# Optimization experiments

Measured on AMD Instinct MI355X. Metric: run time of the kernel, lower is better.

## Reference

```python
import jax, jax.numpy as jnp
import numpy as np
from jax import lax

NOISE_STD = 0.05
TAU = 0.2
B, T, I, H = 16, 512, 8, 256


def setup_inputs() -> dict:
    key = jax.random.key(0)
    ks = jax.random.split(key, 6)
    u = jax.random.normal(ks[0], (B, T, I), dtype=jnp.float32)
    x0 = jnp.zeros((B, H), dtype=jnp.float32)
    noise = jax.random.normal(ks[1], (T, B, H), dtype=jnp.float32)
    # nn.init.normal_(w_hh, std=0.1/H)
    w_hh = jax.random.normal(ks[2], (H, H, H), dtype=jnp.float32) * (0.1 / H)
    # nn.init.normal_(w_in.weight), zero bias
    w_in_w = jax.random.normal(ks[3], (H, I), dtype=jnp.float32)
    w_in_b = jnp.zeros((H,), dtype=jnp.float32)
    # default nn.Linear init for w_out (uniform), approximated with scaled uniform
    bound = 1.0 / np.sqrt(H)
    w_out_w = jax.random.uniform(ks[4], (I, H), dtype=jnp.float32, minval=-bound, maxval=bound)
    w_out_b = jax.random.uniform(ks[5], (I,), dtype=jnp.float32, minval=-bound, maxval=bound)
    return {"u": u, "x0": x0, "noise": noise, "w_hh": w_hh,
            "w_in_w": w_in_w, "w_in_b": w_in_b, "w_out_w": w_out_w, "w_out_b": w_out_b}


def reference(u, x0, noise, w_hh, w_in_w, w_in_b, w_out_w, w_out_b):
    # Precompute input projection for all timesteps: [B,T,H] -> [T,B,H]
    inp = jnp.einsum('bti,hi->tbh', u, w_in_w) + w_in_b

    def step(x, ts):
        u_proj, n_t = ts                     # [B,H], [B,H]
        r = jnp.tanh(x)                      # form='rate'
        # bilinear recurrence: einsum('bj,ijk,bk->bi', r, w_hh, r)
        tmp = jnp.einsum('ijk,bk->bij', w_hh, r)   # [B,H,H]
        rec = jnp.einsum('bj,bij->bi', r, tmp)     # [B,H]
        rec_x = rec + u_proj
        x_new = x + NOISE_STD * n_t + TAU * (-x + rec_x)  # mode='cont'
        return x_new, x_new

    x_last, traj_tb = lax.scan(step, x0, (inp, noise))
    traj = jnp.swapaxes(traj_tb, 0, 1)       # [B,T,H]
    output = jnp.einsum('bth,oh->bto', jnp.tanh(traj), w_out_w) + w_out_b
    return output, x_last, traj
```

## Files before the change

### kernel.cpp

```cpp
#include <hip/hip_runtime.h>
#include <hip/hip_fp16.h>
#include <stdint.h>


#define NOISE_STD 0.05f
#define TAU 0.2f

typedef _Float16 f16x8 __attribute__((ext_vector_type(8)));
typedef float f32x4 __attribute__((ext_vector_type(4)));
typedef unsigned int u32x4 __attribute__((ext_vector_type(4)));

__device__ __forceinline__ float fast_tanh(float x){
  float cx = fminf(fmaxf(x, -10.f), 10.f);
  float e = __expf(2.f*cx);
  return 1.f - 2.f*__builtin_amdgcn_rcpf(e + 1.f);
}

__device__ __forceinline__ void block_sync_lds(){
  asm volatile("s_waitcnt lgkmcnt(0)\n\ts_barrier" ::: "memory");
}

__device__ __forceinline__ unsigned pkmax_u16(unsigned a, unsigned b){
  unsigned d;
  asm("v_pk_max_u16 %0, %1, %2" : "=v"(d) : "v"(a), "v"(b));
  return d;
}

__device__ __forceinline__ bool pair_bad(u32x4 a, u32x4 b){
  unsigned m = pkmax_u16(pkmax_u16(pkmax_u16(a.x, a.y), pkmax_u16(a.z, a.w)),
                         pkmax_u16(pkmax_u16(b.x, b.y), pkmax_u16(b.z, b.w)));
  return ((m & 0xFFFFu) == 0xFFFFu) || ((m >> 16) == 0xFFFFu);
}

__device__ __forceinline__ float row16_sum(float v){
  float s = v; int t;
  t = __builtin_amdgcn_update_dpp(__float_as_int(s), __float_as_int(s), 0x121, 0xF, 0xF, false); s += __int_as_float(t);
  t = __builtin_amdgcn_update_dpp(__float_as_int(s), __float_as_int(s), 0x122, 0xF, 0xF, false); s += __int_as_float(t);
  t = __builtin_amdgcn_update_dpp(__float_as_int(s), __float_as_int(s), 0x124, 0xF, 0xF, false); s += __int_as_float(t);
  t = __builtin_amdgcn_update_dpp(__float_as_int(s), __float_as_int(s), 0x128, 0xF, 0xF, false); s += __int_as_float(t);
  return s;
}

__device__ __forceinline__ unsigned pack2h(float a, float b){
  return (unsigned)__half_as_ushort(__float2half(a)) |
         ((unsigned)__half_as_ushort(__float2half(b)) << 16);
}

__global__ void prep_kernel(const float* __restrict__ u, const float* __restrict__ noise,
                            const float* __restrict__ w_in_w, const float* __restrict__ w_in_b,
                            const float* __restrict__ w_hh,
                            float* __restrict__ pre2, __half* __restrict__ wsw,
                            uint4* __restrict__ rG4, int sent_u4){
  int F = blockIdx.x*256 + threadIdx.x;
  {
    int b = F & 15; int h = (F>>4) & 255; int t = F >> 12;
    const float* up = u + (b*512 + t)*8;
    const float* wp = w_in_w + h*8;
    float s = w_in_b[h];
    #pragma unroll
    for (int i2 = 0; i2 < 8; ++i2) s += up[i2]*wp[i2];
    pre2[h*8192 + t*16 + b] = NOISE_STD*noise[t*4096 + b*256 + h] + TAU*s;
  }
  {
    int lane = F & 63, ks = (F>>6)&7, jtl = (F>>9)&3, wv = (F>>11)&3, i = F>>13;
    int j = (wv*4 + jtl)*16 + (lane & 15);
    int kb = ks*32 + (lane>>4)*8;
    const float4* w4 = (const float4*)(w_hh + i*65536 + j*256 + kb);
    float4 a0 = w4[0], a1 = w4[1];
    uint4 o;
    o.x = pack2h(a0.x, a0.y); o.y = pack2h(a0.z, a0.w);
    o.z = pack2h(a1.x, a1.y); o.w = pack2h(a1.z, a1.w);
    ((uint4*)wsw)[F] = o;
  }
  if (F < sent_u4){
    uint4 s4; s4.x = s4.y = s4.z = s4.w = 0xFFFFFFFFu;
    rG4[F] = s4;
  }
}

__global__ void __launch_bounds__(256, 1) rnn_kernel(
    const float* __restrict__ x0, const float* __restrict__ pre2, const __half* __restrict__ wsw,
    __half* rG, float* __restrict__ traj, float* __restrict__ xlast, int LS)
{
  __shared__ alignas(16) unsigned short r_lds[16*264];
  __shared__ alignas(16) unsigned short rT[256*20];
  __shared__ alignas(16) float pre_lds[8192];
  __shared__ alignas(16) float red[64];

  const int tid = threadIdx.x;
  const int bid = blockIdx.x;
  const int wv = tid >> 6, lane = tid & 63;
  const int q = lane >> 4, col = lane & 15;

  if (wv == 0) __builtin_amdgcn_s_setprio(1);

  uint4 wreg[4][8];
  {
    const uint4* gw = (const uint4*)wsw + (size_t)(bid*4 + wv)*32*64 + lane;
    #pragma unroll
    for (int jtl = 0; jtl < 4; ++jtl)
      #pragma unroll
      for (int ks = 0; ks < 8; ++ks)
        wreg[jtl][ks] = gw[(jtl*8 + ks)*64];
  }

  {
    const float4* ps = (const float4*)(pre2 + bid*8192);
    float4* pl = (float4*)pre_lds;
    #pragma unroll
    for (int c = 0; c < 8; ++c) pl[c*256 + tid] = ps[c*256 + tid];
  }

  float xreg = 0.f;
  if (tid < 16) xreg = x0[tid*256 + bid];
  #pragma unroll
  for (int c = 0; c < 16; ++c){
    unsigned short rv = __half_as_ushort(__float2half(fast_tanh(x0[c*256 + tid])));
    r_lds[c*264 + tid] = rv;
    rT[tid*20 + c]     = rv;
  }
  __syncthreads();

  const int p = tid - 128;

  #pragma unroll 1
  for (int t = 0; t < 512; ++t){
    f32x4 acc[4] = {{0.f,0.f,0.f,0.f},{0.f,0.f,0.f,0.f},{0.f,0.f,0.f,0.f},{0.f,0.f,0.f,0.f}};
    #pragma unroll
    for (int ks = 0; ks < 8; ++ks){
      f16x8 A = *(const f16x8*)(r_lds + col*264 + ks*32 + q*8);
      #pragma unroll
      for (int jtl = 0; jtl < 4; ++jtl){
        union { uint4 u; f16x8 v; } wu; wu.u = wreg[jtl][ks];
        acc[jtl] = __builtin_amdgcn_mfma_f32_16x16x32_f16(A, wu.v, acc[jtl], 0, 0, 0);
      }
    }

    float s[4] = {0.f, 0.f, 0.f, 0.f};
    #pragma unroll
    for (int jtl = 0; jtl < 4; ++jtl){
      int j = (wv*4 + jtl)*16 + col;
      unsigned long long rr = *(const unsigned long long*)&rT[j*20 + q*4];
      unsigned lo = (unsigned)rr, hi = (unsigned)(rr >> 32);
      s[0] += acc[jtl][0] * __half2float(__ushort_as_half((unsigned short)(lo & 0xFFFFu)));
      s[1] += acc[jtl][1] * __half2float(__ushort_as_half((unsigned short)(lo >> 16)));
      s[2] += acc[jtl][2] * __half2float(__ushort_as_half((unsigned short)(hi & 0xFFFFu)));
      s[3] += acc[jtl][3] * __half2float(__ushort_as_half((unsigned short)(hi >> 16)));
    }
    #pragma unroll
    for (int reg = 0; reg < 4; ++reg) s[reg] = row16_sum(s[reg]);
    if (col == 0){
      #pragma unroll
      for (int reg = 0; reg < 4; ++reg) red[(q*4 + reg)*4 + wv] = s[reg];
    }
    block_sync_lds();

    if (tid < 16){
      float4 rr4 = *(const float4*)&red[tid*4];
      float rec = rr4.x + rr4.y + rr4.z + rr4.w;
      float xn = xreg + TAU*(rec - xreg) + pre_lds[t*16 + tid];
      xreg = xn;
      unsigned rv = (unsigned)__half_as_ushort(__float2half(fast_tanh(xn)));
      __half* dst = rG + ((size_t)t*256 + bid)*LS + tid;
      asm volatile("global_store_short %0, %1, off sc1"
                   :: "v"(dst), "v"(rv) : "memory");
      traj[(size_t)tid*131072 + t*256 + bid] = xn;
    }

    if (p >= 0 && t < 511){
      const __half* cp0 = rG + ((size_t)t*256 + 2*p)*LS;
      const __half* cp1 = cp0 + LS;
      u32x4 d0, d1, d2, d3;
      bool needL = true, needH = true;
      __builtin_amdgcn_s_sleep(4);
      for (;;){
        asm volatile("global_load_dwordx4 %0, %4, off sc0 sc1\n\t"
                     "global_load_dwordx4 %1, %4, off offset:16 sc0 sc1\n\t"
                     "global_load_dwordx4 %2, %5, off sc0 sc1\n\t"
                     "global_load_dwordx4 %3, %5, off offset:16 sc0 sc1"
                     : "=&v"(d0), "=&v"(d1), "=&v"(d2), "=&v"(d3)
                     : "v"(cp0), "v"(cp1) : "memory");
        asm volatile("s_waitcnt vmcnt(2)" ::: "memory");
        __builtin_amdgcn_sched_barrier(0);
        if (needL && !pair_bad(d0, d1)){
          union { u32x4 v[2]; unsigned short h[16]; } U; U.v[0] = d0; U.v[1] = d1;
          #pragma unroll
          for (int b = 0; b < 16; ++b) r_lds[b*264 + 2*p] = U.h[b];
          unsigned long long* rp = (unsigned long long*)&rT[(2*p)*20];
          rp[0] = ((unsigned long long)d0.y << 32) | d0.x;
          rp[1] = ((unsigned long long)d0.w << 32) | d0.z;
          rp[2] = ((unsigned long long)d1.y << 32) | d1.x;
          rp[3] = ((unsigned long long)d1.w << 32) | d1.z;
          needL = false;
        }
        asm volatile("s_waitcnt vmcnt(0)" ::: "memory");
        __builtin_amdgcn_sched_barrier(0);
        if (needH && !pair_bad(d2, d3)){
          union { u32x4 v[2]; unsigned short h[16]; } U; U.v[0] = d2; U.v[1] = d3;
          #pragma unroll
          for (int b = 0; b < 16; ++b) r_lds[b*264 + 2*p + 1] = U.h[b];
          unsigned long long* rp = (unsigned long long*)&rT[(2*p + 1)*20];
          rp[0] = ((unsigned long long)d2.y << 32) | d2.x;
          rp[1] = ((unsigned long long)d2.w << 32) | d2.z;
          rp[2] = ((unsigned long long)d3.y << 32) | d3.x;
          rp[3] = ((unsigned long long)d3.w << 32) | d3.z;
          needH = false;
        }
        if (!needL && !needH) break;
        __builtin_amdgcn_s_sleep(1);
      }
    }
    block_sync_lds();
  }
  if (tid < 16) xlast[tid*256 + bid] = xreg;
}

__global__ void out_kernel(const float* __restrict__ traj, const float* __restrict__ w_out_w,
                           const float* __restrict__ w_out_b, float* __restrict__ out){
  __shared__ float wo[2048];
  int tid = threadIdx.x;
  #pragma unroll
  for (int c = 0; c < 8; ++c) wo[c*256 + tid] = w_out_w[c*256 + tid];
  __syncthreads();
  int wv = tid >> 6, lane = tid & 63;
  int p = blockIdx.x*4 + wv;
  float4 v = *(const float4*)&traj[(size_t)p*256 + lane*4];
  float th0 = fast_tanh(v.x), th1 = fast_tanh(v.y), th2 = fast_tanh(v.z), th3 = fast_tanh(v.w);
  #pragma unroll
  for (int o = 0; o < 8; ++o){
    const float* w = &wo[o*256 + lane*4];
    float s = th0*w[0] + th1*w[1] + th2*w[2] + th3*w[3];
    #pragma unroll
    for (int off = 32; off > 0; off >>= 1) s += __shfl_xor(s, off, 64);
    if (lane == 0) out[(size_t)p*8 + o] = s + w_out_b[o];
  }
}

extern "C" void kernel_launch(void* const* d_in, const int* in_sizes, int n_in,
                              void* d_out, int out_size, void* d_ws, size_t ws_size,
                              hipStream_t stream){
  const float* u       = (const float*)d_in[0];
  const float* x0      = (const float*)d_in[1];
  const float* noise   = (const float*)d_in[2];
  const float* w_hh    = (const float*)d_in[3];
  const float* w_in_w  = (const float*)d_in[4];
  const float* w_in_b  = (const float*)d_in[5];
  const float* w_out_w = (const float*)d_in[6];
  const float* w_out_b = (const float*)d_in[7];

  float* out   = (float*)d_out;
  float* xlast = out + 65536;
  float* traj  = xlast + 4096;

  int LS = (ws_size >= (size_t)56*1024*1024) ? 64 : 16;
  size_t rg_bytes = (size_t)512*256*LS*2;

  uint8_t* ws = (uint8_t*)d_ws;
  __half* rG   = (__half*)ws;
  float*  pre2 = (float*)(ws + rg_bytes);
  __half* wsw  = (__half*)(ws + rg_bytes + 8388608);

  prep_kernel<<<8192, 256, 0, stream>>>(u, noise, w_in_w, w_in_b, w_hh,
                                        pre2, wsw, (uint4*)rG, LS*16384);
  {
    void* args[] = {(void*)&x0, (void*)&pre2, (void*)&wsw,
                    (void*)&rG, (void*)&traj, (void*)&xlast, (void*)&LS};
    hipLaunchCooperativeKernel((const void*)rnn_kernel, dim3(256), dim3(256),
                               args, 0, stream);
  }
  out_kernel<<<2048, 256, 0, stream>>>(traj, w_out_w, w_out_b, out);
}
```

Baseline: 1.492 ms.

## Add two-level gather of hidden state through per-group bundler blocks

Each block now writes its tanh output into one of 8 group buffers, laid out contiguously. Blocks 0-7 then poll their group slot and repack it into a compact bundle buffer. Consumer blocks poll the bundled layout instead of 256 scattered padded lines. The goal is to cut the number of distinct cache lines each consumer must spin on across the cooperative grid. The cost is an extra serial hop through the bundler blocks on every timestep's critical path, plus a fixed workspace layout.

```diff
diff --git a/kernel.cpp b/kernel.cpp
--- a/kernel.cpp
+++ b/kernel.cpp
@@ -29,6 +29,11 @@
 __device__ __forceinline__ bool pair_bad(u32x4 a, u32x4 b){
   unsigned m = pkmax_u16(pkmax_u16(pkmax_u16(a.x, a.y), pkmax_u16(a.z, a.w)),
                          pkmax_u16(pkmax_u16(b.x, b.y), pkmax_u16(b.z, b.w)));
+  return ((m & 0xFFFFu) == 0xFFFFu) || ((m >> 16) == 0xFFFFu);
+}
+
+__device__ __forceinline__ bool quad_bad(u32x4 a){
+  unsigned m = pkmax_u16(pkmax_u16(a.x, a.y), pkmax_u16(a.z, a.w));
   return ((m & 0xFFFFu) == 0xFFFFu) || ((m >> 16) == 0xFFFFu);
 }
 
@@ -80,7 +85,7 @@
 
 __global__ void __launch_bounds__(256, 1) rnn_kernel(
     const float* __restrict__ x0, const float* __restrict__ pre2, const __half* __restrict__ wsw,
-    __half* rG, float* __restrict__ traj, float* __restrict__ xlast, int LS)
+    __half* rG, __half* bund, float* __restrict__ traj, float* __restrict__ xlast)
 {
   __shared__ alignas(16) unsigned short r_lds[16*264];
   __shared__ alignas(16) unsigned short rT[256*20];
@@ -91,6 +96,7 @@
   const int bid = blockIdx.x;
   const int wv = tid >> 6, lane = tid & 63;
   const int q = lane >> 4, col = lane & 15;
+  const int grp = bid & 7, mem = bid >> 3;
 
   if (wv == 0) __builtin_amdgcn_s_setprio(1);
 
@@ -161,15 +167,37 @@
       float xn = xreg + TAU*(rec - xreg) + pre_lds[t*16 + tid];
       xreg = xn;
       unsigned rv = (unsigned)__half_as_ushort(__float2half(fast_tanh(xn)));
-      __half* dst = rG + ((size_t)t*256 + bid)*LS + tid;
+      __half* dst = rG + (size_t)(t*8 + grp)*1024 + mem*32 + tid;
       asm volatile("global_store_short %0, %1, off sc1"
                    :: "v"(dst), "v"(rv) : "memory");
       traj[(size_t)tid*131072 + t*256 + bid] = xn;
     }
 
+    if (bid < 8 && wv == 1 && t < 511){
+      int m = lane >> 1, h = lane & 1;
+      const __half* src = rG + (size_t)(t*8 + bid)*1024 + m*32 + h*8;
+      __half* dst = bund + (size_t)(t*8 + bid)*512 + m*16 + h*8;
+      bool done = false;
+      while (!done){
+        u32x4 d;
+        asm volatile("global_load_dwordx4 %0, %1, off sc0 sc1"
+                     : "=&v"(d) : "v"(src) : "memory");
+        asm volatile("s_waitcnt vmcnt(0)" ::: "memory");
+        __builtin_amdgcn_sched_barrier(0);
+        if (!quad_bad(d)){
+          asm volatile("global_store_dwordx4 %0, %1, off sc1"
+                       :: "v"(dst), "v"(d) : "memory");
+          done = true;
+        } else {
+          __builtin_amdgcn_s_sleep(1);
+        }
+      }
+    }
+
     if (p >= 0 && t < 511){
-      const __half* cp0 = rG + ((size_t)t*256 + 2*p)*LS;
-      const __half* cp1 = cp0 + LS;
+      int i0 = 2*p, i1 = 2*p + 1;
+      const __half* cp0 = bund + (size_t)(t*8 + (i0 & 7))*512 + (i0 >> 3)*16;
+      const __half* cp1 = bund + (size_t)(t*8 + (i1 & 7))*512 + (i1 >> 3)*16;
       u32x4 d0, d1, d2, d3;
       bool needL = true, needH = true;
       __builtin_amdgcn_s_sleep(4);
@@ -185,8 +213,8 @@
         if (needL && !pair_bad(d0, d1)){
           union { u32x4 v[2]; unsigned short h[16]; } U; U.v[0] = d0; U.v[1] = d1;
           #pragma unroll
-          for (int b = 0; b < 16; ++b) r_lds[b*264 + 2*p] = U.h[b];
-          unsigned long long* rp = (unsigned long long*)&rT[(2*p)*20];
+          for (int b = 0; b < 16; ++b) r_lds[b*264 + i0] = U.h[b];
+          unsigned long long* rp = (unsigned long long*)&rT[i0*20];
           rp[0] = ((unsigned long long)d0.y << 32) | d0.x;
           rp[1] = ((unsigned long long)d0.w << 32) | d0.z;
           rp[2] = ((unsigned long long)d1.y << 32) | d1.x;
@@ -198,8 +226,8 @@
         if (needH && !pair_bad(d2, d3)){
           union { u32x4 v[2]; unsigned short h[16]; } U; U.v[0] = d2; U.v[1] = d3;
           #pragma unroll
-          for (int b = 0; b < 16; ++b) r_lds[b*264 + 2*p + 1] = U.h[b];
-          unsigned long long* rp = (unsigned long long*)&rT[(2*p + 1)*20];
+          for (int b = 0; b < 16; ++b) r_lds[b*264 + i1] = U.h[b];
+          unsigned long long* rp = (unsigned long long*)&rT[i1*20];
           rp[0] = ((unsigned long long)d2.y << 32) | d2.x;
           rp[1] = ((unsigned long long)d2.w << 32) | d2.z;
           rp[2] = ((unsigned long long)d3.y << 32) | d3.x;
@@ -252,19 +280,17 @@
   float* xlast = out + 65536;
   float* traj  = xlast + 4096;
 
-  int LS = (ws_size >= (size_t)56*1024*1024) ? 64 : 16;
-  size_t rg_bytes = (size_t)512*256*LS*2;
-
   uint8_t* ws = (uint8_t*)d_ws;
   __half* rG   = (__half*)ws;
-  float*  pre2 = (float*)(ws + rg_bytes);
-  __half* wsw  = (__half*)(ws + rg_bytes + 8388608);
+  __half* bund = (__half*)(ws + 8388608);
+  float*  pre2 = (float*)(ws + 8388608 + 4194304);
+  __half* wsw  = (__half*)(ws + 20971520);
 
   prep_kernel<<<8192, 256, 0, stream>>>(u, noise, w_in_w, w_in_b, w_hh,
-                                        pre2, wsw, (uint4*)rG, LS*16384);
+                                        pre2, wsw, (uint4*)rG, 786432);
   {
     void* args[] = {(void*)&x0, (void*)&pre2, (void*)&wsw,
-                    (void*)&rG, (void*)&traj, (void*)&xlast, (void*)&LS};
+                    (void*)&rG, (void*)&bund, (void*)&traj, (void*)&xlast};
     hipLaunchCooperativeKernel((const void*)rnn_kernel, dim3(256), dim3(256),
                                args, 0, stream);
   }
```

Measured after the change: 1.770 ms. +18.7%, slower.

## Spread cross-block state polling over all threads with double-buffered loads

Applied to the files above, without the earlier changes.

The cross-block exchange of tanh(x) values is now polled by all 256 threads, one column each, instead of 128 threads handling two columns each. The polling loop ping-pongs between two in-flight load pairs, so one pair is checked while the next is already requested, which shortens the latency of each poll. The clamp in fast_tanh is also removed to save two instructions per call. The risk is that very large inputs reach the exp without a clamp, although inf and 0 still give ±1, and that doubling the number of polling threads adds more memory traffic.

```diff
diff --git a/kernel.cpp b/kernel.cpp
--- a/kernel.cpp
+++ b/kernel.cpp
@@ -11,8 +11,7 @@
 typedef unsigned int u32x4 __attribute__((ext_vector_type(4)));
 
 __device__ __forceinline__ float fast_tanh(float x){
-  float cx = fminf(fmaxf(x, -10.f), 10.f);
-  float e = __expf(2.f*cx);
+  float e = __expf(2.f*x);
   return 1.f - 2.f*__builtin_amdgcn_rcpf(e + 1.f);
 }
 
@@ -120,8 +119,6 @@
     rT[tid*20 + c]     = rv;
   }
   __syncthreads();
-
-  const int p = tid - 128;
 
   #pragma unroll 1
   for (int t = 0; t < 512; ++t){
@@ -167,48 +164,43 @@
       traj[(size_t)tid*131072 + t*256 + bid] = xn;
     }
 
-    if (p >= 0 && t < 511){
-      const __half* cp0 = rG + ((size_t)t*256 + 2*p)*LS;
-      const __half* cp1 = cp0 + LS;
-      u32x4 d0, d1, d2, d3;
-      bool needL = true, needH = true;
+    if (t < 511){
+      const __half* cp = rG + ((size_t)t*256 + tid)*LS;
+      u32x4 a0, a1, b0, b1;
+      bool inB = false;
       __builtin_amdgcn_s_sleep(4);
+      asm volatile("global_load_dwordx4 %0, %2, off sc0 sc1\n\t"
+                   "global_load_dwordx4 %1, %2, off offset:16 sc0 sc1"
+                   : "=&v"(a0), "=&v"(a1) : "v"(cp) : "memory");
       for (;;){
-        asm volatile("global_load_dwordx4 %0, %4, off sc0 sc1\n\t"
-                     "global_load_dwordx4 %1, %4, off offset:16 sc0 sc1\n\t"
-                     "global_load_dwordx4 %2, %5, off sc0 sc1\n\t"
-                     "global_load_dwordx4 %3, %5, off offset:16 sc0 sc1"
-                     : "=&v"(d0), "=&v"(d1), "=&v"(d2), "=&v"(d3)
-                     : "v"(cp0), "v"(cp1) : "memory");
+        asm volatile("global_load_dwordx4 %0, %2, off sc0 sc1\n\t"
+                     "global_load_dwordx4 %1, %2, off offset:16 sc0 sc1"
+                     : "=&v"(b0), "=&v"(b1) : "v"(cp) : "memory");
         asm volatile("s_waitcnt vmcnt(2)" ::: "memory");
         __builtin_amdgcn_sched_barrier(0);
-        if (needL && !pair_bad(d0, d1)){
-          union { u32x4 v[2]; unsigned short h[16]; } U; U.v[0] = d0; U.v[1] = d1;
-          #pragma unroll
-          for (int b = 0; b < 16; ++b) r_lds[b*264 + 2*p] = U.h[b];
-          unsigned long long* rp = (unsigned long long*)&rT[(2*p)*20];
-          rp[0] = ((unsigned long long)d0.y << 32) | d0.x;
-          rp[1] = ((unsigned long long)d0.w << 32) | d0.z;
-          rp[2] = ((unsigned long long)d1.y << 32) | d1.x;
-          rp[3] = ((unsigned long long)d1.w << 32) | d1.z;
-          needL = false;
-        }
-        asm volatile("s_waitcnt vmcnt(0)" ::: "memory");
+        if (!pair_bad(a0, a1)) { inB = false; break; }
+        __builtin_amdgcn_s_sleep(1);
+        asm volatile("global_load_dwordx4 %0, %2, off sc0 sc1\n\t"
+                     "global_load_dwordx4 %1, %2, off offset:16 sc0 sc1"
+                     : "=&v"(a0), "=&v"(a1) : "v"(cp) : "memory");
+        asm volatile("s_waitcnt vmcnt(2)" ::: "memory");
         __builtin_amdgcn_sched_barrier(0);
-        if (needH && !pair_bad(d2, d3)){
-          union { u32x4 v[2]; unsigned short h[16]; } U; U.v[0] = d2; U.v[1] = d3;
-          #pragma unroll
-          for (int b = 0; b < 16; ++b) r_lds[b*264 + 2*p + 1] = U.h[b];
-          unsigned long long* rp = (unsigned long long*)&rT[(2*p + 1)*20];
-          rp[0] = ((unsigned long long)d2.y << 32) | d2.x;
-          rp[1] = ((unsigned long long)d2.w << 32) | d2.z;
-          rp[2] = ((unsigned long long)d3.y << 32) | d3.x;
-          rp[3] = ((unsigned long long)d3.w << 32) | d3.z;
-          needH = false;
-        }
-        if (!needL && !needH) break;
+        if (!pair_bad(b0, b1)) { inB = true; break; }
         __builtin_amdgcn_s_sleep(1);
       }
+      asm volatile("s_waitcnt vmcnt(0)"
+                   :: "v"(a0), "v"(a1), "v"(b0), "v"(b1) : "memory");
+      __builtin_amdgcn_sched_barrier(0);
+      u32x4 d0 = inB ? b0 : a0;
+      u32x4 d1 = inB ? b1 : a1;
+      union { u32x4 v[2]; unsigned short h[16]; } U; U.v[0] = d0; U.v[1] = d1;
+      #pragma unroll
+      for (int b = 0; b < 16; ++b) r_lds[b*264 + tid] = U.h[b];
+      unsigned long long* rp = (unsigned long long*)&rT[tid*20];
+      rp[0] = ((unsigned long long)d0.y << 32) | d0.x;
+      rp[1] = ((unsigned long long)d0.w << 32) | d0.z;
+      rp[2] = ((unsigned long long)d1.y << 32) | d1.x;
+      rp[3] = ((unsigned long long)d1.w << 32) | d1.z;
     }
     block_sync_lds();
   }
```

Result: slower. 1.636 ms (+9.7%).
